# Kernel optimization log

Hardware: AMD Instinct MI355X
Metric: run time of the kernel (lower is better)

## Reference

```python
import jax, jax.numpy as jnp
import numpy as np


def setup_inputs() -> dict:
    key = jax.random.key(0)
    kq, kv = jax.random.split(key)
    N, To, Ti, H = 8, 1024, 4096, 512
    queries = jax.random.normal(kq, (N, To, H), dtype=jnp.float32)
    values = jax.random.normal(kv, (N, Ti, H), dtype=jnp.float32)
    return {"queries": queries, "values": values}


def reference(queries, values):
    # scores: N x To x Ti (unscaled, unmasked dot-product attention)
    scores = jnp.einsum("noh,nih->noi", queries, values)
    attn = jax.nn.softmax(scores, axis=-1)          # softmax over Ti
    out = jnp.einsum("noi,nih->noh", attn, values)  # N x To x H
    return out, attn
```

## Files before the change

### kernel.cpp

```cpp
#include <hip/hip_runtime.h>
#include <hip/hip_bf16.h>

typedef __bf16 bf16x8 __attribute__((ext_vector_type(8)));
typedef __bf16 bf16x4 __attribute__((ext_vector_type(4)));
typedef float  f32x4  __attribute__((ext_vector_type(4)));

constexpr int N_  = 8;
constexpr int TO_ = 1024;
constexpr int TI_ = 4096;
constexpr int H_  = 512;

__device__ inline void split8(const float4& x0, const float4& x1,
                              bf16x8& h, bf16x8& l)
{
    float xs[8] = {x0.x, x0.y, x0.z, x0.w, x1.x, x1.y, x1.z, x1.w};
#pragma unroll
    for (int i = 0; i < 8; ++i) {
        __bf16 hh = (__bf16)xs[i];
        h[i] = hh;
        l[i] = (__bf16)(xs[i] - (float)hh);
    }
}

__device__ inline void cvt8(const float4& x0, const float4& x1, bf16x8& h)
{
    float xs[8] = {x0.x, x0.y, x0.z, x0.w, x1.x, x1.y, x1.z, x1.w};
#pragma unroll
    for (int i = 0; i < 8; ++i) h[i] = (__bf16)xs[i];
}

__global__ __launch_bounds__(256)
void zero_kernel(float4* __restrict__ p)
{
    p[(size_t)blockIdx.x * 256 + threadIdx.x] = float4{0.f, 0.f, 0.f, 0.f};
}

__global__ __launch_bounds__(256)
void split_kernel(const float* __restrict__ X, __bf16* __restrict__ Xh,
                  __bf16* __restrict__ Xl)
{
    const size_t idx = ((size_t)blockIdx.x * 256 + threadIdx.x) * 8;
    const float4* src = reinterpret_cast<const float4*>(X + idx);
    float4 x0 = src[0], x1 = src[1];
    bf16x8 h, l;
    split8(x0, x1, h, l);
    *reinterpret_cast<bf16x8*>(Xh + idx) = h;
    *reinterpret_cast<bf16x8*>(Xl + idx) = l;
}

__global__ __launch_bounds__(256)
void vt2_kernel(const __bf16* __restrict__ Vh, __bf16* __restrict__ Vt)
{
    const int hb = blockIdx.x, tb = blockIdx.y, n = blockIdx.z;
    const int h  = hb * 64 + (threadIdx.x >> 2);
    const int tq = threadIdx.x & 3;
    const __bf16* Vn = Vh + (size_t)n * TI_ * H_;
    __bf16* Vtn = Vt + (size_t)n * H_ * TI_;

#pragma unroll
    for (int j = 0; j < 16; ++j) {
        const int t0 = tb * 512 + tq * 128 + j * 8;
        bf16x8 o;
#pragma unroll
        for (int e = 0; e < 8; ++e)
            o[e] = Vn[(size_t)(t0 + e) * H_ + h];
        *reinterpret_cast<bf16x8*>(&Vtn[(size_t)h * TI_ + t0]) = o;
    }
}

__global__ __launch_bounds__(256, 2)
void qk3_kernel(const __bf16* __restrict__ Qh, const __bf16* __restrict__ Ql,
                const __bf16* __restrict__ Vh, const __bf16* __restrict__ Vl,
                float* __restrict__ S)
{
    __shared__ __bf16 Ah[128 * 64];
    __shared__ __bf16 Al[128 * 64];
    __shared__ __bf16 Bh[128 * 64];
    __shared__ __bf16 Bl[128 * 64];

    const int tt = blockIdx.x, mt = blockIdx.y, n = blockIdx.z;
    const size_t qoff = ((size_t)n * TO_ + (size_t)mt * 128) * H_;
    const size_t voff = ((size_t)n * TI_ + (size_t)tt * 128) * H_;
    const __bf16* Qhb = Qh + qoff;
    const __bf16* Qlb = Ql + qoff;
    const __bf16* Vhb = Vh + voff;
    const __bf16* Vlb = Vl + voff;

    const int tid  = threadIdx.x;
    const int lane = tid & 63, wave = tid >> 6;
    const int wr = wave >> 1, wc = wave & 1;
    const int fr = lane & 15, fq = lane >> 4;

    const int srow = tid >> 3;
    const int sc   = tid & 7;

    auto stage = [&](const __bf16* __restrict__ g, __bf16* lds, int k0) {
#pragma unroll
        for (int i = 0; i < 4; ++i) {
            const int row = i * 32 + srow;
            const int csw = sc ^ (row & 7);
            const __bf16* gs = g + (size_t)row * H_ + k0 + csw * 8;
            const int q0 = (i * 256 + wave * 64) * 16;
            __builtin_amdgcn_global_load_lds(
                (const __attribute__((address_space(1))) void*)gs,
                (__attribute__((address_space(3))) void*)((char*)lds + q0),
                16, 0, 0);
        }
    };

    f32x4 acc[4][4] = {};

    for (int kt = 0; kt < H_ / 64; ++kt) {
        const int k0 = kt * 64;
        __syncthreads();
        stage(Qhb, Ah, k0);
        stage(Qlb, Al, k0);
        stage(Vhb, Bh, k0);
        stage(Vlb, Bl, k0);
        __syncthreads();

#pragma unroll
        for (int kk = 0; kk < 2; ++kk) {
            bf16x8 ah[4], al[4], bh[4], bl[4];
#pragma unroll
            for (int m = 0; m < 4; ++m) {
                const int row = wr * 64 + m * 16 + fr;
                const int cs  = (kk * 4 + fq) ^ (row & 7);
                ah[m] = *reinterpret_cast<const bf16x8*>(&Ah[row * 64 + cs * 8]);
                al[m] = *reinterpret_cast<const bf16x8*>(&Al[row * 64 + cs * 8]);
            }
#pragma unroll
            for (int j = 0; j < 4; ++j) {
                const int row = wc * 64 + j * 16 + fr;
                const int cs  = (kk * 4 + fq) ^ (row & 7);
                bh[j] = *reinterpret_cast<const bf16x8*>(&Bh[row * 64 + cs * 8]);
                bl[j] = *reinterpret_cast<const bf16x8*>(&Bl[row * 64 + cs * 8]);
            }
#pragma unroll
            for (int m = 0; m < 4; ++m)
#pragma unroll
                for (int j = 0; j < 4; ++j) {
                    acc[m][j] = __builtin_amdgcn_mfma_f32_16x16x32_bf16(ah[m], bh[j], acc[m][j], 0, 0, 0);
                    acc[m][j] = __builtin_amdgcn_mfma_f32_16x16x32_bf16(ah[m], bl[j], acc[m][j], 0, 0, 0);
                    acc[m][j] = __builtin_amdgcn_mfma_f32_16x16x32_bf16(al[m], bh[j], acc[m][j], 0, 0, 0);
                }
        }
    }

    float* Sb = S + ((size_t)n * TO_ + (size_t)mt * 128) * TI_ + (size_t)tt * 128;
    const int crow0 = wr * 64 + fq * 4;
    const int ccol0 = wc * 64 + fr;
#pragma unroll
    for (int m = 0; m < 4; ++m)
#pragma unroll
        for (int j = 0; j < 4; ++j)
#pragma unroll
            for (int r = 0; r < 4; ++r)
                Sb[(size_t)(crow0 + m * 16 + r) * TI_ + (ccol0 + j * 16)] = acc[m][j][r];
}

__global__ __launch_bounds__(256)
void softmax2_kernel(float* __restrict__ S, __bf16* __restrict__ A16)
{
    const int wave = threadIdx.x >> 6, lane = threadIdx.x & 63;
    const size_t row = (size_t)blockIdx.x * 4 + wave;
    float4* p = reinterpret_cast<float4*>(S + row * TI_);
    __bf16* p16 = A16 + row * TI_;

    float4 v[16];
    float m = -3.0e38f;
#pragma unroll
    for (int j = 0; j < 16; ++j) {
        v[j] = p[j * 64 + lane];
        m = fmaxf(m, fmaxf(fmaxf(v[j].x, v[j].y), fmaxf(v[j].z, v[j].w)));
    }
#pragma unroll
    for (int s = 32; s > 0; s >>= 1) m = fmaxf(m, __shfl_xor(m, s));

    constexpr float L2E = 1.4426950408889634f;
    float sum = 0.f;
#pragma unroll
    for (int j = 0; j < 16; ++j) {
        v[j].x = exp2f((v[j].x - m) * L2E);
        v[j].y = exp2f((v[j].y - m) * L2E);
        v[j].z = exp2f((v[j].z - m) * L2E);
        v[j].w = exp2f((v[j].w - m) * L2E);
        sum += (v[j].x + v[j].y) + (v[j].z + v[j].w);
    }
#pragma unroll
    for (int s = 32; s > 0; s >>= 1) sum += __shfl_xor(sum, s);

    const float inv = 1.0f / sum;
#pragma unroll
    for (int j = 0; j < 16; ++j) {
        v[j].x *= inv; v[j].y *= inv; v[j].z *= inv; v[j].w *= inv;
        p[j * 64 + lane] = v[j];
        bf16x4 o;
        o[0] = (__bf16)v[j].x; o[1] = (__bf16)v[j].y;
        o[2] = (__bf16)v[j].z; o[3] = (__bf16)v[j].w;
        *reinterpret_cast<bf16x4*>(&p16[(j * 64 + lane) * 4]) = o;
    }
}

constexpr int VBM = 128, VBN = 256, VBK = 64, VKC = 1024;

__global__ __launch_bounds__(256, 2)
void pv6_kernel(const __bf16* __restrict__ A16, const __bf16* __restrict__ Vt,
                float* __restrict__ O)
{
    __shared__ __bf16 Asm[VBM * VBK];
    __shared__ __bf16 Bsm[VBN * VBK];

    const int flat = blockIdx.x;
    const int mt = flat >> 6;
    const int g  = flat & 63;
    const int n  = g >> 3;
    const int ht = (g >> 2) & 1;
    const int kc = g & 3;

    const __bf16* Ab = A16 + ((size_t)n * TO_ + (size_t)mt * VBM) * TI_ + (size_t)kc * VKC;
    const __bf16* Bb = Vt  + ((size_t)n * H_  + (size_t)ht * VBN) * TI_ + (size_t)kc * VKC;

    const int tid = threadIdx.x, lane = tid & 63, wave = tid >> 6;
    const int wm = wave >> 1, wh = wave & 1;
    const int fr = lane & 15, fq = lane >> 4;

    f32x4 acc[4][8] = {};

    for (int kt = 0; kt < VKC / VBK; ++kt) {
        const int k0 = kt * VBK;
        __syncthreads();

#pragma unroll
        for (int i = 0; i < 4; ++i) {
            const int q   = i * 256 + tid;
            const int row = q >> 3, c = q & 7;
            const int csw = c ^ (row & 7);
            const __bf16* gs = Ab + (size_t)row * TI_ + k0 + csw * 8;
            const int q0 = i * 256 + wave * 64;
            __builtin_amdgcn_global_load_lds(
                (const __attribute__((address_space(1))) void*)gs,
                (__attribute__((address_space(3))) void*)((char*)Asm + q0 * 16),
                16, 0, 0);
        }
#pragma unroll
        for (int i = 0; i < 8; ++i) {
            const int q   = i * 256 + tid;
            const int row = q >> 3, c = q & 7;
            const int csw = c ^ (row & 7);
            const __bf16* gs = Bb + (size_t)row * TI_ + k0 + csw * 8;
            const int q0 = i * 256 + wave * 64;
            __builtin_amdgcn_global_load_lds(
                (const __attribute__((address_space(1))) void*)gs,
                (__attribute__((address_space(3))) void*)((char*)Bsm + q0 * 16),
                16, 0, 0);
        }
        __syncthreads();

#pragma unroll
        for (int kk = 0; kk < 2; ++kk) {
            bf16x8 a[4], b[8];
#pragma unroll
            for (int m = 0; m < 4; ++m) {
                const int row = wm * 64 + m * 16 + fr;
                const int cph = (kk * 4 + fq) ^ (row & 7);
                a[m] = *reinterpret_cast<const bf16x8*>(
                    (const char*)Asm + row * 128 + cph * 16);
            }
#pragma unroll
            for (int j = 0; j < 8; ++j) {
                const int row = wh * 128 + j * 16 + fr;
                const int cph = (kk * 4 + fq) ^ (row & 7);
                b[j] = *reinterpret_cast<const bf16x8*>(
                    (const char*)Bsm + row * 128 + cph * 16);
            }
#pragma unroll
            for (int m = 0; m < 4; ++m)
#pragma unroll
                for (int j = 0; j < 8; ++j)
                    acc[m][j] = __builtin_amdgcn_mfma_f32_16x16x32_bf16(
                        a[m], b[j], acc[m][j], 0, 0, 0);
        }
    }

    float* Ob = O + ((size_t)n * TO_ + (size_t)mt * VBM) * H_ + ht * VBN;
#pragma unroll
    for (int m = 0; m < 4; ++m) {
        const int orow = wm * 64 + m * 16 + fq * 4;
#pragma unroll
        for (int j = 0; j < 8; ++j) {
            const int ocol = wh * 128 + j * 16 + fr;
#pragma unroll
            for (int r = 0; r < 4; ++r)
                atomicAdd(&Ob[(size_t)(orow + r) * H_ + ocol], acc[m][j][r]);
        }
    }
}

constexpr int BM1 = 128, BN1 = 128, BK1 = 32, LP1 = BK1 + 8;

__global__ __launch_bounds__(256, 2)
void qk_kernel(const float* __restrict__ Q, const float* __restrict__ V,
               float* __restrict__ S)
{
    __shared__ __bf16 Ah[BM1 * LP1];
    __shared__ __bf16 Al[BM1 * LP1];
    __shared__ __bf16 Bh[BN1 * LP1];
    __shared__ __bf16 Bl[BN1 * LP1];

    const int tt = blockIdx.x, mt = blockIdx.y, n = blockIdx.z;
    const float* Qb = Q + ((size_t)n * TO_ + (size_t)mt * BM1) * H_;
    const float* Vb = V + ((size_t)n * TI_ + (size_t)tt * BN1) * H_;

    const int tid  = threadIdx.x;
    const int lane = tid & 63, wave = tid >> 6;
    const int wr = wave >> 1, wc = wave & 1;
    const int srow = tid >> 2, scg = tid & 3;

    f32x4 acc[4][4] = {};

    for (int k0 = 0; k0 < H_; k0 += BK1) {
        __syncthreads();
#pragma unroll
        for (int half = 0; half < 2; ++half) {
            const int r = srow + half * 64;
            {
                const float4* src =
                    reinterpret_cast<const float4*>(Qb + (size_t)r * H_ + k0 + scg * 8);
                float4 x0 = src[0], x1 = src[1];
                bf16x8 hv, lv;
                split8(x0, x1, hv, lv);
                *reinterpret_cast<bf16x8*>(&Ah[r * LP1 + scg * 8]) = hv;
                *reinterpret_cast<bf16x8*>(&Al[r * LP1 + scg * 8]) = lv;
            }
            {
                const float4* src =
                    reinterpret_cast<const float4*>(Vb + (size_t)r * H_ + k0 + scg * 8);
                float4 x0 = src[0], x1 = src[1];
                bf16x8 hv, lv;
                split8(x0, x1, hv, lv);
                *reinterpret_cast<bf16x8*>(&Bh[r * LP1 + scg * 8]) = hv;
                *reinterpret_cast<bf16x8*>(&Bl[r * LP1 + scg * 8]) = lv;
            }
        }
        __syncthreads();

        bf16x8 ah[4], al[4], bh[4], bl[4];
        const int fr = lane & 15, fg = (lane >> 4) * 8;
#pragma unroll
        for (int m = 0; m < 4; ++m) {
            const int row = wr * 64 + m * 16 + fr;
            ah[m] = *reinterpret_cast<const bf16x8*>(&Ah[row * LP1 + fg]);
            al[m] = *reinterpret_cast<const bf16x8*>(&Al[row * LP1 + fg]);
        }
#pragma unroll
        for (int j = 0; j < 4; ++j) {
            const int row = wc * 64 + j * 16 + fr;
            bh[j] = *reinterpret_cast<const bf16x8*>(&Bh[row * LP1 + fg]);
            bl[j] = *reinterpret_cast<const bf16x8*>(&Bl[row * LP1 + fg]);
        }
#pragma unroll
        for (int m = 0; m < 4; ++m)
#pragma unroll
            for (int j = 0; j < 4; ++j) {
                acc[m][j] = __builtin_amdgcn_mfma_f32_16x16x32_bf16(ah[m], bh[j], acc[m][j], 0, 0, 0);
                acc[m][j] = __builtin_amdgcn_mfma_f32_16x16x32_bf16(ah[m], bl[j], acc[m][j], 0, 0, 0);
                acc[m][j] = __builtin_amdgcn_mfma_f32_16x16x32_bf16(al[m], bh[j], acc[m][j], 0, 0, 0);
            }
    }

    float* Sb = S + ((size_t)n * TO_ + (size_t)mt * BM1) * TI_ + (size_t)tt * BN1;
    const int crow0 = wr * 64 + (lane >> 4) * 4;
    const int ccol0 = wc * 64 + (lane & 15);
#pragma unroll
    for (int m = 0; m < 4; ++m)
#pragma unroll
        for (int j = 0; j < 4; ++j)
#pragma unroll
            for (int r = 0; r < 4; ++r)
                Sb[(size_t)(crow0 + m * 16 + r) * TI_ + (ccol0 + j * 16)] = acc[m][j][r];
}

__global__ __launch_bounds__(256)
void softmax_kernel(float* __restrict__ S)
{
    const int wave = threadIdx.x >> 6, lane = threadIdx.x & 63;
    const size_t row = (size_t)blockIdx.x * 4 + wave;
    float4* p = reinterpret_cast<float4*>(S + row * TI_);

    float4 v[16];
    float m = -3.0e38f;
#pragma unroll
    for (int j = 0; j < 16; ++j) {
        v[j] = p[j * 64 + lane];
        m = fmaxf(m, fmaxf(fmaxf(v[j].x, v[j].y), fmaxf(v[j].z, v[j].w)));
    }
#pragma unroll
    for (int s = 32; s > 0; s >>= 1) m = fmaxf(m, __shfl_xor(m, s));

    constexpr float L2E = 1.4426950408889634f;
    float sum = 0.f;
#pragma unroll
    for (int j = 0; j < 16; ++j) {
        v[j].x = exp2f((v[j].x - m) * L2E);
        v[j].y = exp2f((v[j].y - m) * L2E);
        v[j].z = exp2f((v[j].z - m) * L2E);
        v[j].w = exp2f((v[j].w - m) * L2E);
        sum += (v[j].x + v[j].y) + (v[j].z + v[j].w);
    }
#pragma unroll
    for (int s = 32; s > 0; s >>= 1) sum += __shfl_xor(sum, s);

    const float inv = 1.0f / sum;
#pragma unroll
    for (int j = 0; j < 16; ++j) {
        v[j].x *= inv; v[j].y *= inv; v[j].z *= inv; v[j].w *= inv;
        p[j * 64 + lane] = v[j];
    }
}

__global__ __launch_bounds__(256)
void vt_kernel(const float* __restrict__ V, __bf16* __restrict__ Vt)
{
    const int hb = blockIdx.x, tb = blockIdx.y, n = blockIdx.z;
    const int h  = hb * 64 + (threadIdx.x >> 2);
    const int tq = threadIdx.x & 3;
    const float* Vn = V + (size_t)n * TI_ * H_;
    __bf16* Vtn = Vt + (size_t)n * H_ * TI_;

#pragma unroll
    for (int j = 0; j < 16; ++j) {
        const int t0 = tb * 512 + tq * 128 + j * 8;
        bf16x8 o;
#pragma unroll
        for (int e = 0; e < 8; ++e)
            o[e] = (__bf16)Vn[(size_t)(t0 + e) * H_ + h];
        *reinterpret_cast<bf16x8*>(&Vtn[(size_t)h * TI_ + t0]) = o;
    }
}

constexpr int PBM = 32, PBK = 64, PLP = PBK + 8;

__global__ __launch_bounds__(512, 2)
void pv_fast_kernel(const float* __restrict__ A, const __bf16* __restrict__ Vt,
                    float* __restrict__ O)
{
    __shared__ __bf16 AsmF[PBM * PLP];
    __shared__ __bf16 BsmF[512 * PLP];

    const int n = blockIdx.x, mt = blockIdx.y;
    const float*  Ab = A  + ((size_t)n * TO_ + (size_t)mt * PBM) * TI_;
    const __bf16* Vb = Vt + (size_t)n * H_ * TI_;

    const int tid = threadIdx.x, lane = tid & 63, wv = tid >> 6;
    const int ar = tid >> 4;
    const int ac = (tid & 15) * 4;
    const int bh = tid >> 3;
    const int bc = (tid & 7) * 8;

    float4 aReg;
    bf16x8 bReg[8];

    auto loadTile = [&](int k0) {
        aReg = *reinterpret_cast<const float4*>(Ab + (size_t)ar * TI_ + k0 + ac);
#pragma unroll
        for (int i = 0; i < 8; ++i)
            bReg[i] = *reinterpret_cast<const bf16x8*>(
                Vb + (size_t)(bh + i * 64) * TI_ + k0 + bc);
    };

    f32x4 acc[2][4] = {};
    const int fr = lane & 15, fg = (lane >> 4) * 8;

    loadTile(0);
    constexpr int NT = TI_ / PBK;
    for (int kt = 0; kt < NT; ++kt) {
        __syncthreads();
        {
            bf16x4 av;
            av[0] = (__bf16)aReg.x; av[1] = (__bf16)aReg.y;
            av[2] = (__bf16)aReg.z; av[3] = (__bf16)aReg.w;
            *reinterpret_cast<bf16x4*>(&AsmF[ar * PLP + ac]) = av;
#pragma unroll
            for (int i = 0; i < 8; ++i)
                *reinterpret_cast<bf16x8*>(&BsmF[(bh + i * 64) * PLP + bc]) = bReg[i];
        }
        __syncthreads();
        if (kt + 1 < NT) loadTile((kt + 1) * PBK);

#pragma unroll
        for (int kk = 0; kk < 2; ++kk) {
            bf16x8 af[2], bfr[4];
#pragma unroll
            for (int m = 0; m < 2; ++m)
                af[m] = *reinterpret_cast<const bf16x8*>(
                    &AsmF[(m * 16 + fr) * PLP + kk * 32 + fg]);
#pragma unroll
            for (int j = 0; j < 4; ++j)
                bfr[j] = *reinterpret_cast<const bf16x8*>(
                    &BsmF[(wv * 64 + j * 16 + fr) * PLP + kk * 32 + fg]);
#pragma unroll
            for (int m = 0; m < 2; ++m)
#pragma unroll
                for (int j = 0; j < 4; ++j)
                    acc[m][j] = __builtin_amdgcn_mfma_f32_16x16x32_bf16(
                        af[m], bfr[j], acc[m][j], 0, 0, 0);
        }
    }

    float* Ob = O + ((size_t)n * TO_ + (size_t)mt * PBM) * H_ + wv * 64;
    const int crow = (lane >> 4) * 4;
    const int ccol = lane & 15;
#pragma unroll
    for (int m = 0; m < 2; ++m)
#pragma unroll
        for (int j = 0; j < 4; ++j)
#pragma unroll
            for (int r = 0; r < 4; ++r)
                Ob[(size_t)(m * 16 + crow + r) * H_ + j * 16 + ccol] = acc[m][j][r];
}

extern "C" void kernel_launch(void* const* d_in, const int* in_sizes, int n_in,
                              void* d_out, int out_size, void* d_ws, size_t ws_size,
                              hipStream_t stream)
{
    const float* Q = (const float*)d_in[0];
    const float* V = (const float*)d_in[1];
    float* out  = (float*)d_out;
    float* attn = out + (size_t)N_ * TO_ * H_;

    const size_t NV = (size_t)N_ * TI_ * H_;
    const size_t NQ = (size_t)N_ * TO_ * H_;
    const size_t FULL_BYTES = (3 * NV + 2 * NQ) * sizeof(__bf16);
    const size_t VT_BYTES   = NV * sizeof(__bf16);

    __bf16* wsb = (__bf16*)d_ws;
    __bf16* Vt = wsb;
    __bf16* Vh = wsb + NV;
    __bf16* Vl = wsb + 2 * NV;
    __bf16* Qh = wsb + 3 * NV;
    __bf16* Ql = wsb + 3 * NV + NQ;
    __bf16* A16 = wsb + NV;

    if (ws_size >= FULL_BYTES) {
        zero_kernel<<<dim3((unsigned)(NQ / 4 / 256)), 256, 0, stream>>>((float4*)out);
        split_kernel<<<dim3(NV / (256 * 8)), 256, 0, stream>>>(V, Vh, Vl);
        split_kernel<<<dim3(NQ / (256 * 8)), 256, 0, stream>>>(Q, Qh, Ql);
        vt2_kernel<<<dim3(H_ / 64, TI_ / 512, N_), 256, 0, stream>>>(Vh, Vt);
        qk3_kernel<<<dim3(TI_ / 128, TO_ / 128, N_), 256, 0, stream>>>(Qh, Ql, Vh, Vl, attn);
        softmax2_kernel<<<dim3(N_ * TO_ / 4), 256, 0, stream>>>(attn, A16);
        pv6_kernel<<<dim3(512), 256, 0, stream>>>(A16, Vt, out);
    } else if (ws_size >= VT_BYTES) {
        vt_kernel<<<dim3(H_ / 64, TI_ / 512, N_), 256, 0, stream>>>(V, Vt);
        qk_kernel<<<dim3(TI_ / BN1, TO_ / BM1, N_), 256, 0, stream>>>(Q, V, attn);
        softmax_kernel<<<dim3(N_ * TO_ / 4), 256, 0, stream>>>(attn);
        pv_fast_kernel<<<dim3(N_, TO_ / PBM), 512, 0, stream>>>(attn, Vt, out);
    }
}
```

Before: 284.3 us.

## Double-buffer QK and PV GEMMs with 512 threads; replace atomics with split-K partials

The QK kernel moves to 512 threads per block with double-buffered LDS tiles, so the global-to-LDS load for the next K step overlaps MFMA work on the current one. The PV kernel is also double-buffered with 512 threads, and its K split drops from 4 to 2. The two partial sums are written with plain stores to the output and to a workspace buffer, then combined by a separate add kernel. This removes the zero-fill kernel and the float atomics, at the cost of one extra elementwise pass, doubled LDS use and possible occupancy limits.

```diff
diff --git a/kernel.cpp b/kernel.cpp
--- a/kernel.cpp
+++ b/kernel.cpp
@@ -20,19 +20,6 @@
         h[i] = hh;
         l[i] = (__bf16)(xs[i] - (float)hh);
     }
-}
-
-__device__ inline void cvt8(const float4& x0, const float4& x1, bf16x8& h)
-{
-    float xs[8] = {x0.x, x0.y, x0.z, x0.w, x1.x, x1.y, x1.z, x1.w};
-#pragma unroll
-    for (int i = 0; i < 8; ++i) h[i] = (__bf16)xs[i];
-}
-
-__global__ __launch_bounds__(256)
-void zero_kernel(float4* __restrict__ p)
-{
-    p[(size_t)blockIdx.x * 256 + threadIdx.x] = float4{0.f, 0.f, 0.f, 0.f};
 }
 
 __global__ __launch_bounds__(256)
@@ -68,15 +55,15 @@
     }
 }
 
-__global__ __launch_bounds__(256, 2)
-void qk3_kernel(const __bf16* __restrict__ Qh, const __bf16* __restrict__ Ql,
+__global__ __launch_bounds__(512, 2)
+void qk4_kernel(const __bf16* __restrict__ Qh, const __bf16* __restrict__ Ql,
                 const __bf16* __restrict__ Vh, const __bf16* __restrict__ Vl,
                 float* __restrict__ S)
 {
-    __shared__ __bf16 Ah[128 * 64];
-    __shared__ __bf16 Al[128 * 64];
-    __shared__ __bf16 Bh[128 * 64];
-    __shared__ __bf16 Bl[128 * 64];
+    __shared__ __bf16 AhA[128 * 64], AhB[128 * 64];
+    __shared__ __bf16 AlA[128 * 64], AlB[128 * 64];
+    __shared__ __bf16 BhA[128 * 64], BhB[128 * 64];
+    __shared__ __bf16 BlA[128 * 64], BlB[128 * 64];
 
     const int tt = blockIdx.x, mt = blockIdx.y, n = blockIdx.z;
     const size_t qoff = ((size_t)n * TO_ + (size_t)mt * 128) * H_;
@@ -88,43 +75,40 @@
 
     const int tid  = threadIdx.x;
     const int lane = tid & 63, wave = tid >> 6;
-    const int wr = wave >> 1, wc = wave & 1;
+    const int wm = wave >> 1, wc = wave & 1;
     const int fr = lane & 15, fq = lane >> 4;
 
-    const int srow = tid >> 3;
-    const int sc   = tid & 7;
-
-    auto stage = [&](const __bf16* __restrict__ g, __bf16* lds, int k0) {
-#pragma unroll
-        for (int i = 0; i < 4; ++i) {
-            const int row = i * 32 + srow;
-            const int csw = sc ^ (row & 7);
+    auto stage1 = [&](const __bf16* __restrict__ g, __bf16* lds, int k0) {
+#pragma unroll
+        for (int i = 0; i < 2; ++i) {
+            const int q   = i * 512 + tid;
+            const int row = q >> 3, c = q & 7;
+            const int csw = c ^ (row & 7);
             const __bf16* gs = g + (size_t)row * H_ + k0 + csw * 8;
-            const int q0 = (i * 256 + wave * 64) * 16;
+            const int q0 = (i * 512 + wave * 64) * 16;
             __builtin_amdgcn_global_load_lds(
                 (const __attribute__((address_space(1))) void*)gs,
                 (__attribute__((address_space(3))) void*)((char*)lds + q0),
                 16, 0, 0);
         }
     };
-
-    f32x4 acc[4][4] = {};
-
-    for (int kt = 0; kt < H_ / 64; ++kt) {
-        const int k0 = kt * 64;
-        __syncthreads();
-        stage(Qhb, Ah, k0);
-        stage(Qlb, Al, k0);
-        stage(Vhb, Bh, k0);
-        stage(Vlb, Bl, k0);
-        __syncthreads();
-
+    auto stage = [&](__bf16* ah, __bf16* al, __bf16* bh, __bf16* bl, int k0) {
+        stage1(Qhb, ah, k0);
+        stage1(Qlb, al, k0);
+        stage1(Vhb, bh, k0);
+        stage1(Vlb, bl, k0);
+    };
+
+    f32x4 acc[2][4] = {};
+
+    auto compute = [&](const __bf16* Ah, const __bf16* Al,
+                       const __bf16* Bh, const __bf16* Bl) {
 #pragma unroll
         for (int kk = 0; kk < 2; ++kk) {
-            bf16x8 ah[4], al[4], bh[4], bl[4];
-#pragma unroll
-            for (int m = 0; m < 4; ++m) {
-                const int row = wr * 64 + m * 16 + fr;
+            bf16x8 ah[2], al[2], bh[4], bl[4];
+#pragma unroll
+            for (int m = 0; m < 2; ++m) {
+                const int row = wm * 32 + m * 16 + fr;
                 const int cs  = (kk * 4 + fq) ^ (row & 7);
                 ah[m] = *reinterpret_cast<const bf16x8*>(&Ah[row * 64 + cs * 8]);
                 al[m] = *reinterpret_cast<const bf16x8*>(&Al[row * 64 + cs * 8]);
@@ -137,7 +121,7 @@
                 bl[j] = *reinterpret_cast<const bf16x8*>(&Bl[row * 64 + cs * 8]);
             }
 #pragma unroll
-            for (int m = 0; m < 4; ++m)
+            for (int m = 0; m < 2; ++m)
 #pragma unroll
                 for (int j = 0; j < 4; ++j) {
                     acc[m][j] = __builtin_amdgcn_mfma_f32_16x16x32_bf16(ah[m], bh[j], acc[m][j], 0, 0, 0);
@@ -145,13 +129,25 @@
                     acc[m][j] = __builtin_amdgcn_mfma_f32_16x16x32_bf16(al[m], bh[j], acc[m][j], 0, 0, 0);
                 }
         }
+    };
+
+    constexpr int NT = H_ / 64;
+    stage(AhA, AlA, BhA, BlA, 0);
+    __syncthreads();
+    for (int kt = 0; kt < NT; kt += 2) {
+        if (kt + 1 < NT) stage(AhB, AlB, BhB, BlB, (kt + 1) * 64);
+        compute(AhA, AlA, BhA, BlA);
+        __syncthreads();
+        if (kt + 2 < NT) stage(AhA, AlA, BhA, BlA, (kt + 2) * 64);
+        compute(AhB, AlB, BhB, BlB);
+        __syncthreads();
     }
 
     float* Sb = S + ((size_t)n * TO_ + (size_t)mt * 128) * TI_ + (size_t)tt * 128;
-    const int crow0 = wr * 64 + fq * 4;
+    const int crow0 = wm * 32 + fq * 4;
     const int ccol0 = wc * 64 + fr;
 #pragma unroll
-    for (int m = 0; m < 4; ++m)
+    for (int m = 0; m < 2; ++m)
 #pragma unroll
         for (int j = 0; j < 4; ++j)
 #pragma unroll
@@ -202,99 +198,115 @@
     }
 }
 
-constexpr int VBM = 128, VBN = 256, VBK = 64, VKC = 1024;
-
-__global__ __launch_bounds__(256, 2)
-void pv6_kernel(const __bf16* __restrict__ A16, const __bf16* __restrict__ Vt,
-                float* __restrict__ O)
-{
-    __shared__ __bf16 Asm[VBM * VBK];
-    __shared__ __bf16 Bsm[VBN * VBK];
+__global__ __launch_bounds__(512, 2)
+void pv7_kernel(const __bf16* __restrict__ A16, const __bf16* __restrict__ Vt,
+                float* __restrict__ O, float* __restrict__ P)
+{
+    __shared__ __bf16 AsmA[128 * 64], AsmB[128 * 64];
+    __shared__ __bf16 BsmA[256 * 64], BsmB[256 * 64];
 
     const int flat = blockIdx.x;
-    const int mt = flat >> 6;
-    const int g  = flat & 63;
-    const int n  = g >> 3;
-    const int ht = (g >> 2) & 1;
-    const int kc = g & 3;
-
-    const __bf16* Ab = A16 + ((size_t)n * TO_ + (size_t)mt * VBM) * TI_ + (size_t)kc * VKC;
-    const __bf16* Bb = Vt  + ((size_t)n * H_  + (size_t)ht * VBN) * TI_ + (size_t)kc * VKC;
+    const int mt = flat >> 5;
+    const int g  = flat & 31;
+    const int n  = g >> 2;
+    const int ht = (g >> 1) & 1;
+    const int kc = g & 1;
+
+    const __bf16* Ab = A16 + ((size_t)n * TO_ + (size_t)mt * 128) * TI_ + (size_t)kc * 2048;
+    const __bf16* Bb = Vt  + ((size_t)n * H_  + (size_t)ht * 256) * TI_ + (size_t)kc * 2048;
 
     const int tid = threadIdx.x, lane = tid & 63, wave = tid >> 6;
-    const int wm = wave >> 1, wh = wave & 1;
+    const int wm = wave >> 2, wh = wave & 3;
     const int fr = lane & 15, fq = lane >> 4;
 
-    f32x4 acc[4][8] = {};
-
-    for (int kt = 0; kt < VKC / VBK; ++kt) {
-        const int k0 = kt * VBK;
-        __syncthreads();
-
-#pragma unroll
-        for (int i = 0; i < 4; ++i) {
-            const int q   = i * 256 + tid;
+    auto stage = [&](__bf16* asm_, __bf16* bsm_, int k0) {
+#pragma unroll
+        for (int i = 0; i < 2; ++i) {
+            const int q   = i * 512 + tid;
             const int row = q >> 3, c = q & 7;
             const int csw = c ^ (row & 7);
             const __bf16* gs = Ab + (size_t)row * TI_ + k0 + csw * 8;
-            const int q0 = i * 256 + wave * 64;
+            const int q0 = (i * 512 + wave * 64) * 16;
             __builtin_amdgcn_global_load_lds(
                 (const __attribute__((address_space(1))) void*)gs,
-                (__attribute__((address_space(3))) void*)((char*)Asm + q0 * 16),
+                (__attribute__((address_space(3))) void*)((char*)asm_ + q0),
                 16, 0, 0);
         }
 #pragma unroll
-        for (int i = 0; i < 8; ++i) {
-            const int q   = i * 256 + tid;
+        for (int i = 0; i < 4; ++i) {
+            const int q   = i * 512 + tid;
             const int row = q >> 3, c = q & 7;
             const int csw = c ^ (row & 7);
             const __bf16* gs = Bb + (size_t)row * TI_ + k0 + csw * 8;
-            const int q0 = i * 256 + wave * 64;
+            const int q0 = (i * 512 + wave * 64) * 16;
             __builtin_amdgcn_global_load_lds(
                 (const __attribute__((address_space(1))) void*)gs,
-                (__attribute__((address_space(3))) void*)((char*)Bsm + q0 * 16),
+                (__attribute__((address_space(3))) void*)((char*)bsm_ + q0),
                 16, 0, 0);
         }
-        __syncthreads();
-
+    };
+
+    f32x4 acc[4][4] = {};
+
+    auto compute = [&](const __bf16* Asm, const __bf16* Bsm) {
 #pragma unroll
         for (int kk = 0; kk < 2; ++kk) {
-            bf16x8 a[4], b[8];
+            bf16x8 a[4], b[4];
 #pragma unroll
             for (int m = 0; m < 4; ++m) {
                 const int row = wm * 64 + m * 16 + fr;
-                const int cph = (kk * 4 + fq) ^ (row & 7);
-                a[m] = *reinterpret_cast<const bf16x8*>(
-                    (const char*)Asm + row * 128 + cph * 16);
-            }
-#pragma unroll
-            for (int j = 0; j < 8; ++j) {
-                const int row = wh * 128 + j * 16 + fr;
-                const int cph = (kk * 4 + fq) ^ (row & 7);
-                b[j] = *reinterpret_cast<const bf16x8*>(
-                    (const char*)Bsm + row * 128 + cph * 16);
+                const int cs  = (kk * 4 + fq) ^ (row & 7);
+                a[m] = *reinterpret_cast<const bf16x8*>(&Asm[row * 64 + cs * 8]);
+            }
+#pragma unroll
+            for (int j = 0; j < 4; ++j) {
+                const int row = wh * 64 + j * 16 + fr;
+                const int cs  = (kk * 4 + fq) ^ (row & 7);
+                b[j] = *reinterpret_cast<const bf16x8*>(&Bsm[row * 64 + cs * 8]);
             }
 #pragma unroll
             for (int m = 0; m < 4; ++m)
 #pragma unroll
-                for (int j = 0; j < 8; ++j)
+                for (int j = 0; j < 4; ++j)
                     acc[m][j] = __builtin_amdgcn_mfma_f32_16x16x32_bf16(
                         a[m], b[j], acc[m][j], 0, 0, 0);
         }
-    }
-
-    float* Ob = O + ((size_t)n * TO_ + (size_t)mt * VBM) * H_ + ht * VBN;
+    };
+
+    constexpr int NT = 2048 / 64;
+    stage(AsmA, BsmA, 0);
+    __syncthreads();
+    for (int kt = 0; kt < NT; kt += 2) {
+        if (kt + 1 < NT) stage(AsmB, BsmB, (kt + 1) * 64);
+        compute(AsmA, BsmA);
+        __syncthreads();
+        if (kt + 2 < NT) stage(AsmA, BsmA, (kt + 2) * 64);
+        compute(AsmB, BsmB);
+        __syncthreads();
+    }
+
+    float* D  = (kc == 0) ? O : P;
+    float* Db = D + ((size_t)n * TO_ + (size_t)mt * 128) * H_ + ht * 256;
 #pragma unroll
     for (int m = 0; m < 4; ++m) {
         const int orow = wm * 64 + m * 16 + fq * 4;
 #pragma unroll
-        for (int j = 0; j < 8; ++j) {
-            const int ocol = wh * 128 + j * 16 + fr;
+        for (int j = 0; j < 4; ++j) {
+            const int ocol = wh * 64 + j * 16 + fr;
 #pragma unroll
             for (int r = 0; r < 4; ++r)
-                atomicAdd(&Ob[(size_t)(orow + r) * H_ + ocol], acc[m][j][r]);
-        }
-    }
+                Db[(size_t)(orow + r) * H_ + ocol] = acc[m][j][r];
+        }
+    }
+}
+
+__global__ __launch_bounds__(256)
+void add_kernel(float4* __restrict__ o, const float4* __restrict__ p)
+{
+    const size_t i = (size_t)blockIdx.x * 256 + threadIdx.x;
+    float4 a = o[i], b = p[i];
+    a.x += b.x; a.y += b.y; a.z += b.z; a.w += b.w;
+    o[i] = a;
 }
 
 constexpr int BM1 = 128, BN1 = 128, BK1 = 32, LP1 = BK1 + 8;
@@ -541,15 +553,17 @@
     __bf16* Qh = wsb + 3 * NV;
     __bf16* Ql = wsb + 3 * NV + NQ;
     __bf16* A16 = wsb + NV;
+    float*  Ppart = (float*)(wsb + 3 * NV);
 
     if (ws_size >= FULL_BYTES) {
-        zero_kernel<<<dim3((unsigned)(NQ / 4 / 256)), 256, 0, stream>>>((float4*)out);
         split_kernel<<<dim3(NV / (256 * 8)), 256, 0, stream>>>(V, Vh, Vl);
         split_kernel<<<dim3(NQ / (256 * 8)), 256, 0, stream>>>(Q, Qh, Ql);
         vt2_kernel<<<dim3(H_ / 64, TI_ / 512, N_), 256, 0, stream>>>(Vh, Vt);
-        qk3_kernel<<<dim3(TI_ / 128, TO_ / 128, N_), 256, 0, stream>>>(Qh, Ql, Vh, Vl, attn);
+        qk4_kernel<<<dim3(TI_ / 128, TO_ / 128, N_), 512, 0, stream>>>(Qh, Ql, Vh, Vl, attn);
         softmax2_kernel<<<dim3(N_ * TO_ / 4), 256, 0, stream>>>(attn, A16);
-        pv6_kernel<<<dim3(512), 256, 0, stream>>>(A16, Vt, out);
+        pv7_kernel<<<dim3(256), 512, 0, stream>>>(A16, Vt, out, Ppart);
+        add_kernel<<<dim3((unsigned)(NQ / 4 / 256)), 256, 0, stream>>>(
+            (float4*)out, (const float4*)Ppart);
     } else if (ws_size >= VT_BYTES) {
         vt_kernel<<<dim3(H_ / 64, TI_ / 512, N_), 256, 0, stream>>>(V, Vt);
         qk_kernel<<<dim3(TI_ / BN1, TO_ / BM1, N_), 256, 0, stream>>>(Q, V, attn);
```

New measurement: 262.6 us. -7.6%, faster.

## Fuse V split with transpose and replace atomic PV reduction with two-way partial sums

Applied to the files above, without the earlier changes.

The separate V split and transpose kernels are merged into one pass that reads fp32 V and writes the hi, lo and transposed hi copies, which removes a round trip through the bf16 intermediate. The PV GEMM is retiled to 128x128 output tiles with a two-way K split. Each half writes plain stores into either the output or a workspace partial buffer, and a small add kernel then combines them. This replaces the zero-fill kernel and the fp32 atomics. The fused split kernel does strided scalar reads and writes of Vh and Vl, which may coalesce less well than the old vectorized split.

```diff
diff --git a/kernel.cpp b/kernel.cpp
--- a/kernel.cpp
+++ b/kernel.cpp
@@ -20,19 +20,6 @@
         h[i] = hh;
         l[i] = (__bf16)(xs[i] - (float)hh);
     }
-}
-
-__device__ inline void cvt8(const float4& x0, const float4& x1, bf16x8& h)
-{
-    float xs[8] = {x0.x, x0.y, x0.z, x0.w, x1.x, x1.y, x1.z, x1.w};
-#pragma unroll
-    for (int i = 0; i < 8; ++i) h[i] = (__bf16)xs[i];
-}
-
-__global__ __launch_bounds__(256)
-void zero_kernel(float4* __restrict__ p)
-{
-    p[(size_t)blockIdx.x * 256 + threadIdx.x] = float4{0.f, 0.f, 0.f, 0.f};
 }
 
 __global__ __launch_bounds__(256)
@@ -49,22 +36,31 @@
 }
 
 __global__ __launch_bounds__(256)
-void vt2_kernel(const __bf16* __restrict__ Vh, __bf16* __restrict__ Vt)
+void splitv_kernel(const float* __restrict__ V, __bf16* __restrict__ Vh,
+                   __bf16* __restrict__ Vl, __bf16* __restrict__ Vt)
 {
     const int hb = blockIdx.x, tb = blockIdx.y, n = blockIdx.z;
     const int h  = hb * 64 + (threadIdx.x >> 2);
     const int tq = threadIdx.x & 3;
-    const __bf16* Vn = Vh + (size_t)n * TI_ * H_;
+    const float* Vn = V + (size_t)n * TI_ * H_;
+    __bf16* Vhn = Vh + (size_t)n * TI_ * H_;
+    __bf16* Vln = Vl + (size_t)n * TI_ * H_;
     __bf16* Vtn = Vt + (size_t)n * H_ * TI_;
 
 #pragma unroll
     for (int j = 0; j < 16; ++j) {
         const int t0 = tb * 512 + tq * 128 + j * 8;
-        bf16x8 o;
-#pragma unroll
-        for (int e = 0; e < 8; ++e)
-            o[e] = Vn[(size_t)(t0 + e) * H_ + h];
-        *reinterpret_cast<bf16x8*>(&Vtn[(size_t)h * TI_ + t0]) = o;
+        bf16x8 oh;
+#pragma unroll
+        for (int e = 0; e < 8; ++e) {
+            const size_t o = (size_t)(t0 + e) * H_ + h;
+            const float x = Vn[o];
+            __bf16 hh = (__bf16)x;
+            oh[e] = hh;
+            Vhn[o] = hh;
+            Vln[o] = (__bf16)(x - (float)hh);
+        }
+        *reinterpret_cast<bf16x8*>(&Vtn[(size_t)h * TI_ + t0]) = oh;
     }
 }
 
@@ -202,99 +198,99 @@
     }
 }
 
-constexpr int VBM = 128, VBN = 256, VBK = 64, VKC = 1024;
-
 __global__ __launch_bounds__(256, 2)
-void pv6_kernel(const __bf16* __restrict__ A16, const __bf16* __restrict__ Vt,
-                float* __restrict__ O)
-{
-    __shared__ __bf16 Asm[VBM * VBK];
-    __shared__ __bf16 Bsm[VBN * VBK];
+void pv8_kernel(const __bf16* __restrict__ A16, const __bf16* __restrict__ Vt,
+                float* __restrict__ O, float* __restrict__ P)
+{
+    __shared__ __bf16 Asm[128 * 64];
+    __shared__ __bf16 Bsm[128 * 64];
 
     const int flat = blockIdx.x;
-    const int mt = flat >> 6;
-    const int g  = flat & 63;
-    const int n  = g >> 3;
-    const int ht = (g >> 2) & 1;
-    const int kc = g & 3;
-
-    const __bf16* Ab = A16 + ((size_t)n * TO_ + (size_t)mt * VBM) * TI_ + (size_t)kc * VKC;
-    const __bf16* Bb = Vt  + ((size_t)n * H_  + (size_t)ht * VBN) * TI_ + (size_t)kc * VKC;
+    const int n  = flat & 7;
+    const int r  = flat >> 3;
+    const int mt = r & 7;
+    const int ht = (r >> 3) & 3;
+    const int kc = (r >> 5) & 1;
+
+    const __bf16* Ab = A16 + ((size_t)n * TO_ + (size_t)mt * 128) * TI_ + (size_t)kc * 2048;
+    const __bf16* Bb = Vt  + ((size_t)n * H_  + (size_t)ht * 128) * TI_ + (size_t)kc * 2048;
 
     const int tid = threadIdx.x, lane = tid & 63, wave = tid >> 6;
     const int wm = wave >> 1, wh = wave & 1;
     const int fr = lane & 15, fq = lane >> 4;
 
-    f32x4 acc[4][8] = {};
-
-    for (int kt = 0; kt < VKC / VBK; ++kt) {
-        const int k0 = kt * VBK;
-        __syncthreads();
-
+    const int srow = tid >> 3;
+    const int sc   = tid & 7;
+
+    auto stage = [&](const __bf16* __restrict__ g, __bf16* lds, int k0) {
 #pragma unroll
         for (int i = 0; i < 4; ++i) {
-            const int q   = i * 256 + tid;
-            const int row = q >> 3, c = q & 7;
-            const int csw = c ^ (row & 7);
-            const __bf16* gs = Ab + (size_t)row * TI_ + k0 + csw * 8;
-            const int q0 = i * 256 + wave * 64;
+            const int row = i * 32 + srow;
+            const int csw = sc ^ (row & 7);
+            const __bf16* gs = g + (size_t)row * TI_ + k0 + csw * 8;
+            const int q0 = (i * 256 + wave * 64) * 16;
             __builtin_amdgcn_global_load_lds(
                 (const __attribute__((address_space(1))) void*)gs,
-                (__attribute__((address_space(3))) void*)((char*)Asm + q0 * 16),
+                (__attribute__((address_space(3))) void*)((char*)lds + q0),
                 16, 0, 0);
         }
-#pragma unroll
-        for (int i = 0; i < 8; ++i) {
-            const int q   = i * 256 + tid;
-            const int row = q >> 3, c = q & 7;
-            const int csw = c ^ (row & 7);
-            const __bf16* gs = Bb + (size_t)row * TI_ + k0 + csw * 8;
-            const int q0 = i * 256 + wave * 64;
-            __builtin_amdgcn_global_load_lds(
-                (const __attribute__((address_space(1))) void*)gs,
-                (__attribute__((address_space(3))) void*)((char*)Bsm + q0 * 16),
-                16, 0, 0);
-        }
+    };
+
+    f32x4 acc[4][4] = {};
+
+    for (int kt = 0; kt < 2048 / 64; ++kt) {
+        const int k0 = kt * 64;
+        __syncthreads();
+        stage(Ab, Asm, k0);
+        stage(Bb, Bsm, k0);
         __syncthreads();
 
 #pragma unroll
         for (int kk = 0; kk < 2; ++kk) {
-            bf16x8 a[4], b[8];
+            bf16x8 a[4], b[4];
 #pragma unroll
             for (int m = 0; m < 4; ++m) {
                 const int row = wm * 64 + m * 16 + fr;
-                const int cph = (kk * 4 + fq) ^ (row & 7);
-                a[m] = *reinterpret_cast<const bf16x8*>(
-                    (const char*)Asm + row * 128 + cph * 16);
-            }
-#pragma unroll
-            for (int j = 0; j < 8; ++j) {
-                const int row = wh * 128 + j * 16 + fr;
-                const int cph = (kk * 4 + fq) ^ (row & 7);
-                b[j] = *reinterpret_cast<const bf16x8*>(
-                    (const char*)Bsm + row * 128 + cph * 16);
+                const int cs  = (kk * 4 + fq) ^ (row & 7);
+                a[m] = *reinterpret_cast<const bf16x8*>(&Asm[row * 64 + cs * 8]);
+            }
+#pragma unroll
+            for (int j = 0; j < 4; ++j) {
+                const int row = wh * 64 + j * 16 + fr;
+                const int cs  = (kk * 4 + fq) ^ (row & 7);
+                b[j] = *reinterpret_cast<const bf16x8*>(&Bsm[row * 64 + cs * 8]);
             }
 #pragma unroll
             for (int m = 0; m < 4; ++m)
 #pragma unroll
-                for (int j = 0; j < 8; ++j)
+                for (int j = 0; j < 4; ++j)
                     acc[m][j] = __builtin_amdgcn_mfma_f32_16x16x32_bf16(
                         a[m], b[j], acc[m][j], 0, 0, 0);
         }
     }
 
-    float* Ob = O + ((size_t)n * TO_ + (size_t)mt * VBM) * H_ + ht * VBN;
+    float* D  = (kc == 0) ? O : P;
+    float* Db = D + ((size_t)n * TO_ + (size_t)mt * 128) * H_ + ht * 128;
 #pragma unroll
     for (int m = 0; m < 4; ++m) {
         const int orow = wm * 64 + m * 16 + fq * 4;
 #pragma unroll
-        for (int j = 0; j < 8; ++j) {
-            const int ocol = wh * 128 + j * 16 + fr;
-#pragma unroll
-            for (int r = 0; r < 4; ++r)
-                atomicAdd(&Ob[(size_t)(orow + r) * H_ + ocol], acc[m][j][r]);
-        }
-    }
+        for (int j = 0; j < 4; ++j) {
+            const int ocol = wh * 64 + j * 16 + fr;
+#pragma unroll
+            for (int r2 = 0; r2 < 4; ++r2)
+                Db[(size_t)(orow + r2) * H_ + ocol] = acc[m][j][r2];
+        }
+    }
+}
+
+__global__ __launch_bounds__(256)
+void add_kernel(float4* __restrict__ o, const float4* __restrict__ p)
+{
+    const size_t i = (size_t)blockIdx.x * 256 + threadIdx.x;
+    float4 a = o[i], b = p[i];
+    a.x += b.x; a.y += b.y; a.z += b.z; a.w += b.w;
+    o[i] = a;
 }
 
 constexpr int BM1 = 128, BN1 = 128, BK1 = 32, LP1 = BK1 + 8;
@@ -541,15 +537,16 @@
     __bf16* Qh = wsb + 3 * NV;
     __bf16* Ql = wsb + 3 * NV + NQ;
     __bf16* A16 = wsb + NV;
+    float*  Ppart = (float*)(wsb + 3 * NV);
 
     if (ws_size >= FULL_BYTES) {
-        zero_kernel<<<dim3((unsigned)(NQ / 4 / 256)), 256, 0, stream>>>((float4*)out);
-        split_kernel<<<dim3(NV / (256 * 8)), 256, 0, stream>>>(V, Vh, Vl);
+        splitv_kernel<<<dim3(H_ / 64, TI_ / 512, N_), 256, 0, stream>>>(V, Vh, Vl, Vt);
         split_kernel<<<dim3(NQ / (256 * 8)), 256, 0, stream>>>(Q, Qh, Ql);
-        vt2_kernel<<<dim3(H_ / 64, TI_ / 512, N_), 256, 0, stream>>>(Vh, Vt);
         qk3_kernel<<<dim3(TI_ / 128, TO_ / 128, N_), 256, 0, stream>>>(Qh, Ql, Vh, Vl, attn);
         softmax2_kernel<<<dim3(N_ * TO_ / 4), 256, 0, stream>>>(attn, A16);
-        pv6_kernel<<<dim3(512), 256, 0, stream>>>(A16, Vt, out);
+        pv8_kernel<<<dim3(512), 256, 0, stream>>>(A16, Vt, out, Ppart);
+        add_kernel<<<dim3((unsigned)(NQ / 4 / 256)), 256, 0, stream>>>(
+            (float4*)out, (const float4*)Ppart);
     } else if (ws_size >= VT_BYTES) {
         vt_kernel<<<dim3(H_ / 64, TI_ / 512, N_), 256, 0, stream>>>(V, Vt);
         qk_kernel<<<dim3(TI_ / BN1, TO_ / BM1, N_), 256, 0, stream>>>(Q, V, attn);
```

Measured after the change: 280.8 us. No clear change (-1.2%).
